# Optimization experiments

Hardware: AMD Instinct MI355X
Metric: run time of the kernel (lower is better)

The kernel has to match this reference:

```python
import jax, jax.numpy as jnp
import numpy as np

EPS = 1e-5  # torch BatchNorm1d default

def _silu(x):
    return x * jax.nn.sigmoid(x)

def _bn(x, g, b, rm, rv, axis):
    # eval-mode batchnorm along given channel axis
    shape = [1] * x.ndim
    shape[axis] = -1
    return (x - rm.reshape(shape)) * (g.reshape(shape) / jnp.sqrt(rv.reshape(shape) + EPS)) + b.reshape(shape)

def setup_inputs() -> dict:
    key = jax.random.key(0)
    ks = jax.random.split(key, 12)
    b, n, p, d, r = 64, 256, 12, 128, 2
    x = jax.random.normal(ks[0], (b, n, p, d), dtype=jnp.float32)
    # k branch: Conv1d(p -> 1, k=1, bias=False) + BN(1)
    wk = jax.random.normal(ks[1], (p,), dtype=jnp.float32) / np.sqrt(p)
    bn_k_g = jax.random.uniform(ks[2], (1,), dtype=jnp.float32, minval=0.5, maxval=1.5)
    bn_k_b = 0.1 * jax.random.normal(ks[3], (1,), dtype=jnp.float32)
    bn_k_rm = jnp.zeros((1,), jnp.float32)
    bn_k_rv = jnp.ones((1,), jnp.float32)
    # v branch: Conv1d(d -> d, k=1, bias=False) + BN(d)
    wv = jax.random.normal(ks[4], (d, d), dtype=jnp.float32) / np.sqrt(d)
    bn_v_g = jax.random.uniform(ks[5], (d,), dtype=jnp.float32, minval=0.5, maxval=1.5)
    bn_v_b = 0.1 * jax.random.normal(ks[6], (d,), dtype=jnp.float32)
    bn_v_rm = jnp.zeros((d,), jnp.float32)
    bn_v_rv = jnp.ones((d,), jnp.float32)
    # fc_avg / fc_max: Linear(n, n//r, bias=False) -> GELU -> Linear(n//r, n, bias=False)
    w_avg1 = jax.random.normal(ks[7], (n // r, n), dtype=jnp.float32) / np.sqrt(n)
    w_avg2 = jax.random.normal(ks[8], (n, n // r), dtype=jnp.float32) / np.sqrt(n // r)
    w_max1 = jax.random.normal(ks[9], (n // r, n), dtype=jnp.float32) / np.sqrt(n)
    w_max2 = jax.random.normal(ks[10], (n, n // r), dtype=jnp.float32) / np.sqrt(n // r)
    return dict(x=x, wk=wk, bn_k_g=bn_k_g, bn_k_b=bn_k_b, bn_k_rm=bn_k_rm, bn_k_rv=bn_k_rv,
                wv=wv, bn_v_g=bn_v_g, bn_v_b=bn_v_b, bn_v_rm=bn_v_rm, bn_v_rv=bn_v_rv,
                w_avg1=w_avg1, w_avg2=w_avg2, w_max1=w_max1, w_max2=w_max2)

def _forward(x, wk, bn_k_g, bn_k_b, bn_k_rm, bn_k_rv, wv, bn_v_g, bn_v_b, bn_v_rm, bn_v_rv,
             w_avg1, w_avg2, w_max1, w_max2):
    b, n, p, d = x.shape
    xf = x.reshape(b * n, p, d)
    # squeeze-excite gates: pool over d, FC over n
    avg = jnp.mean(xf, axis=-1).reshape(b, n, p).transpose(0, 2, 1)  # [b,p,n]
    mx = jnp.max(xf, axis=-1).reshape(b, n, p).transpose(0, 2, 1)    # [b,p,n]
    gelu = lambda t: jax.nn.gelu(t, approximate=False)
    avg_g = jax.nn.sigmoid(gelu(avg @ w_avg1.T) @ w_avg2.T).transpose(0, 2, 1)  # [b,n,p]
    max_g = jax.nn.sigmoid(gelu(mx @ w_max1.T) @ w_max2.T).transpose(0, 2, 1)   # [b,n,p]
    # k: 1x1 conv over p channels -> [bn, d], BN(1ch), SiLU, softmax over d
    k_raw = jnp.einsum('bpd,p->bd', xf, wk)
    k = jax.nn.softmax(_silu(k_raw * (bn_k_g / jnp.sqrt(bn_k_rv + EPS)) - bn_k_rm * (bn_k_g / jnp.sqrt(bn_k_rv + EPS)) + bn_k_b), axis=-1)  # [bn,d]
    # v: 1x1 conv over d channels on [bn,d,p], BN(d), SiLU -> [bn,p,d]
    v_raw = jnp.einsum('bpd,ed->bpe', xf, wv)  # channel axis is last here
    v = _silu(_bn(v_raw, bn_v_g, bn_v_b, bn_v_rm, bn_v_rv, axis=2))  # [bn,p,d]
    # y = v @ k : [bn,p];  y_pool = (max+avg) @ v : [bn,d]
    y = jnp.einsum('bpd,bd->bp', v, k)
    pool = (max_g + avg_g).reshape(b * n, p)
    y_pool = jnp.einsum('bp,bpd->bd', pool, v)
    out = y_pool[:, None, :] * y[:, :, None]  # [bn,p,d]
    return out.reshape(b, n, p, d)

def reference(x, wk, bn_k_g, bn_k_b, bn_k_rm, bn_k_rv, wv, bn_v_g, bn_v_b, bn_v_rm, bn_v_rv,
              w_avg1, w_avg2, w_max1, w_max2):
    return _forward(x, wk, bn_k_g, bn_k_b, bn_k_rm, bn_k_rv, wv, bn_v_g, bn_v_b, bn_v_rm, bn_v_rv,
                    w_avg1, w_avg2, w_max1, w_max2)
```

## Files before the change

### kernel.cpp

```cpp
#include <hip/hip_runtime.h>
#include <hip/hip_bf16.h>

#define B_   64
#define N_   256
#define P_   12
#define D_   128
#define BN_  (B_*N_)
#define EPSV 1e-5f

typedef float  f32x4  __attribute__((ext_vector_type(4)));
typedef __bf16 bf16x8 __attribute__((ext_vector_type(8)));
typedef __bf16 bf16x4 __attribute__((ext_vector_type(4)));

__device__ float  g_avg[768*256];
__device__ float  g_mx [768*256];
__device__ float  g_h1 [1536*128];
__device__ float  g_pool[BN_*P_];
__device__ float  g_k  [BN_*D_];
__device__ __bf16 g_xbf[(size_t)BN_*P_*D_];
__device__ __align__(16) __bf16 g_wvbf[128*128];
__device__ float  g_tv [128];

__device__ inline float sigm_(float x) { return 1.0f / (1.0f + __expf(-x)); }

__device__ inline float dot4_(float4 a, float4 b, float acc) {
  acc = fmaf(a.x, b.x, acc); acc = fmaf(a.y, b.y, acc);
  acc = fmaf(a.z, b.z, acc); acc = fmaf(a.w, b.w, acc);
  return acc;
}

__global__ __launch_bounds__(256) void k0_prep(const float* __restrict__ wv,
                                               const float* __restrict__ vg,
                                               const float* __restrict__ vb,
                                               const float* __restrict__ vrm,
                                               const float* __restrict__ vrv) {
  int t = blockIdx.x * 256 + threadIdx.x;
  if (blockIdx.x == 0 && threadIdx.x < 128) {
    float s0 = vg[threadIdx.x] * rsqrtf(vrv[threadIdx.x] + EPSV);
    g_tv[threadIdx.x] = vb[threadIdx.x] - vrm[threadIdx.x] * s0;
  }
  int idx = t * 4;
  int e = idx >> 7, d0 = idx & 127;
  float s = vg[e] * rsqrtf(vrv[e] + EPSV);
  bf16x4 h;
#pragma unroll
  for (int j = 0; j < 4; ++j) h[j] = (__bf16)(wv[e * 128 + d0 + j] * s);
  *(bf16x4*)(g_wvbf + idx) = h;
}

__global__ __launch_bounds__(256) void k1_pool(const float* __restrict__ x,
                                               const float* __restrict__ wk,
                                               const float* __restrict__ kg,
                                               const float* __restrict__ kb,
                                               const float* __restrict__ krm,
                                               const float* __restrict__ krv) {
  int w = threadIdx.x >> 6, l = threadIdx.x & 63;
  int bn = blockIdx.x * 4 + w;
  const float* xp = x + (size_t)bn * (P_ * D_);
  __bf16* xbp = g_xbf + (size_t)bn * (P_ * D_);
  int half = l >> 5, lane32 = l & 31;
  float ksc = kg[0] * rsqrtf(krv[0] + EPSV);
  float kbs = kb[0] - krm[0] * ksc;
  float s6[6], m6[6];
  float kr0 = 0, kr1 = 0, kr2 = 0, kr3 = 0;
#pragma unroll
  for (int pp = 0; pp < 6; ++pp) {
    int p = pp * 2 + half;
    float4 v = *(const float4*)(xp + p * D_ + lane32 * 4);
    bf16x4 h;
    h[0] = (__bf16)v.x; h[1] = (__bf16)v.y; h[2] = (__bf16)v.z; h[3] = (__bf16)v.w;
    *(bf16x4*)(xbp + p * D_ + lane32 * 4) = h;
    float wkp = wk[p];
    kr0 = fmaf(v.x, wkp, kr0); kr1 = fmaf(v.y, wkp, kr1);
    kr2 = fmaf(v.z, wkp, kr2); kr3 = fmaf(v.w, wkp, kr3);
    float s = (v.x + v.y) + (v.z + v.w);
    float m = fmaxf(fmaxf(v.x, v.y), fmaxf(v.z, v.w));
#pragma unroll
    for (int off = 16; off; off >>= 1) {
      s += __shfl_xor(s, off);
      m = fmaxf(m, __shfl_xor(m, off));
    }
    s6[pp] = s * (1.0f / D_);
    m6[pp] = m;
  }
  kr0 += __shfl_xor(kr0, 32); kr1 += __shfl_xor(kr1, 32);
  kr2 += __shfl_xor(kr2, 32); kr3 += __shfl_xor(kr3, 32);
  float z0 = kr0 * ksc + kbs, z1 = kr1 * ksc + kbs;
  float z2 = kr2 * ksc + kbs, z3 = kr3 * ksc + kbs;
  z0 = z0 * sigm_(z0); z1 = z1 * sigm_(z1);
  z2 = z2 * sigm_(z2); z3 = z3 * sigm_(z3);
  float mx = fmaxf(fmaxf(z0, z1), fmaxf(z2, z3));
#pragma unroll
  for (int off = 16; off; off >>= 1) mx = fmaxf(mx, __shfl_xor(mx, off));
  float e0 = __expf(z0 - mx), e1 = __expf(z1 - mx);
  float e2 = __expf(z2 - mx), e3 = __expf(z3 - mx);
  float es = (e0 + e1) + (e2 + e3);
#pragma unroll
  for (int off = 16; off; off >>= 1) es += __shfl_xor(es, off);
  float inv = 1.0f / es;
  if (half == 0) {
    float4 kk; kk.x = e0 * inv; kk.y = e1 * inv; kk.z = e2 * inv; kk.w = e3 * inv;
    *(float4*)(g_k + (size_t)bn * D_ + lane32 * 4) = kk;
  }
  if (lane32 == 0) {
    int b = bn >> 8, n = bn & 255;
#pragma unroll
    for (int pp = 0; pp < 6; ++pp) {
      int p = pp * 2 + half;
      g_avg[(b * P_ + p) * N_ + n] = s6[pp];
      g_mx [(b * P_ + p) * N_ + n] = m6[pp];
    }
  }
}

__global__ __launch_bounds__(256) void k2_l1(const float* __restrict__ w_avg1,
                                             const float* __restrict__ w_max1) {
  __shared__ float in_t[16 * 256];
  __shared__ float w_t[64 * 68];
  int t = threadIdx.x;
  int rblk = blockIdx.x % 96, cblk = blockIdx.x / 96;
  int rr0 = rblk * 16, c0 = cblk * 64;
  bool mxb = (rr0 >= 768);
  int r768 = mxb ? rr0 - 768 : rr0;
  const float* in = (mxb ? g_mx : g_avg) + (size_t)r768 * 256;
  const float* w1 = mxb ? w_max1 : w_avg1;
#pragma unroll
  for (int i = 0; i < 4; ++i) {
    int F = t + i * 256, r = F >> 6, k4 = F & 63;
    *(float4*)(in_t + r * 256 + k4 * 4) = *(const float4*)(in + r * 256 + k4 * 4);
  }
  int c = t & 63, rq = t >> 6;
  float a0 = 0, a1 = 0, a2 = 0, a3 = 0;
  for (int kc = 0; kc < 4; ++kc) {
    __syncthreads();
#pragma unroll
    for (int i = 0; i < 4; ++i) {
      int F = t + i * 256, cr = F >> 4, k4 = F & 15;
      *(float4*)(w_t + cr * 68 + k4 * 4) =
          *(const float4*)(w1 + (size_t)(c0 + cr) * 256 + kc * 64 + k4 * 4);
    }
    __syncthreads();
#pragma unroll
    for (int k4 = 0; k4 < 16; ++k4) {
      float4 wv4 = *(float4*)(w_t + c * 68 + k4 * 4);
      a0 = dot4_(*(float4*)(in_t + (rq * 4 + 0) * 256 + kc * 64 + k4 * 4), wv4, a0);
      a1 = dot4_(*(float4*)(in_t + (rq * 4 + 1) * 256 + kc * 64 + k4 * 4), wv4, a1);
      a2 = dot4_(*(float4*)(in_t + (rq * 4 + 2) * 256 + kc * 64 + k4 * 4), wv4, a2);
      a3 = dot4_(*(float4*)(in_t + (rq * 4 + 3) * 256 + kc * 64 + k4 * 4), wv4, a3);
    }
  }
  float accs[4] = {a0, a1, a2, a3};
#pragma unroll
  for (int r = 0; r < 4; ++r) {
    float a = accs[r];
    float g = 0.5f * a * (1.0f + erff(a * 0.70710678f));
    g_h1[(size_t)(rr0 + rq * 4 + r) * 128 + c0 + c] = g;
  }
}

__global__ __launch_bounds__(256) void k2_l2(const float* __restrict__ w_avg2,
                                             const float* __restrict__ w_max2) {
  __shared__ float ina_t[16 * 128];
  __shared__ float inm_t[16 * 128];
  __shared__ float wa_t[64 * 68];
  __shared__ float wm_t[64 * 68];
  int t = threadIdx.x;
  int rblk = blockIdx.x % 48, cblk = blockIdx.x / 48;
  int rr0 = rblk * 16, n0 = cblk * 64;
#pragma unroll
  for (int i = 0; i < 2; ++i) {
    int F = t + i * 256, r = F >> 5, k4 = F & 31;
    *(float4*)(ina_t + r * 128 + k4 * 4) = *(const float4*)(g_h1 + (size_t)(rr0 + r) * 128 + k4 * 4);
    *(float4*)(inm_t + r * 128 + k4 * 4) = *(const float4*)(g_h1 + (size_t)(768 + rr0 + r) * 128 + k4 * 4);
  }
  int c = t & 63, rq = t >> 6;
  float aa0=0, aa1=0, aa2=0, aa3=0, am0=0, am1=0, am2=0, am3=0;
  for (int kc = 0; kc < 2; ++kc) {
    __syncthreads();
#pragma unroll
    for (int i = 0; i < 4; ++i) {
      int F = t + i * 256, cr = F >> 4, k4 = F & 15;
      *(float4*)(wa_t + cr * 68 + k4 * 4) =
          *(const float4*)(w_avg2 + (size_t)(n0 + cr) * 128 + kc * 64 + k4 * 4);
      *(float4*)(wm_t + cr * 68 + k4 * 4) =
          *(const float4*)(w_max2 + (size_t)(n0 + cr) * 128 + kc * 64 + k4 * 4);
    }
    __syncthreads();
#pragma unroll
    for (int k4 = 0; k4 < 16; ++k4) {
      float4 wa4 = *(float4*)(wa_t + c * 68 + k4 * 4);
      float4 wm4 = *(float4*)(wm_t + c * 68 + k4 * 4);
      float4 i0 = *(float4*)(ina_t + (rq * 4 + 0) * 128 + kc * 64 + k4 * 4);
      float4 i1 = *(float4*)(ina_t + (rq * 4 + 1) * 128 + kc * 64 + k4 * 4);
      float4 i2 = *(float4*)(ina_t + (rq * 4 + 2) * 128 + kc * 64 + k4 * 4);
      float4 i3 = *(float4*)(ina_t + (rq * 4 + 3) * 128 + kc * 64 + k4 * 4);
      aa0 = dot4_(i0, wa4, aa0); aa1 = dot4_(i1, wa4, aa1);
      aa2 = dot4_(i2, wa4, aa2); aa3 = dot4_(i3, wa4, aa3);
      float4 j0 = *(float4*)(inm_t + (rq * 4 + 0) * 128 + kc * 64 + k4 * 4);
      float4 j1 = *(float4*)(inm_t + (rq * 4 + 1) * 128 + kc * 64 + k4 * 4);
      float4 j2 = *(float4*)(inm_t + (rq * 4 + 2) * 128 + kc * 64 + k4 * 4);
      float4 j3 = *(float4*)(inm_t + (rq * 4 + 3) * 128 + kc * 64 + k4 * 4);
      am0 = dot4_(j0, wm4, am0); am1 = dot4_(j1, wm4, am1);
      am2 = dot4_(j2, wm4, am2); am3 = dot4_(j3, wm4, am3);
    }
  }
  float va[4] = {aa0, aa1, aa2, aa3};
  float vm[4] = {am0, am1, am2, am3};
#pragma unroll
  for (int r = 0; r < 4; ++r) {
    int rr = rr0 + rq * 4 + r;
    int b = rr / 12, p = rr % 12;
    float pv = sigm_(va[r]) + sigm_(vm[r]);
    g_pool[((size_t)b * 256 + (n0 + c)) * 12 + p] = pv;
  }
}

__global__ __launch_bounds__(64) void k3_main(float* __restrict__ out) {
  int l = threadIdx.x;
  int bcol = l & 15;
  int arow = bcol > 11 ? 11 : bcol;
  int ak = (l >> 4) * 8;
  int p0 = (l >> 4) * 4;
  bool rows_ok = (p0 < 12);

  bf16x8 bfr[8][4];
#pragma unroll
  for (int nt = 0; nt < 8; ++nt) {
    const __bf16* wp = g_wvbf + (bcol + nt * 16) * 128 + ak;
#pragma unroll
    for (int ks = 0; ks < 4; ++ks)
      bfr[nt][ks] = *(const bf16x8*)(wp + ks * 32);
  }
  float tv_e[8];
#pragma unroll
  for (int nt = 0; nt < 8; ++nt) tv_e[nt] = g_tv[bcol + nt * 16];

  for (int it = 0; it < 4; ++it) {
    int bn = blockIdx.x * 4 + it;

    const __bf16* xp = g_xbf + (size_t)bn * (P_ * D_) + arow * D_;
    bf16x8 afr[4];
#pragma unroll
    for (int ks = 0; ks < 4; ++ks) afr[ks] = *(const bf16x8*)(xp + ks * 32 + ak);
    const float* kp = g_k + (size_t)bn * D_;
    float k_e[8];
#pragma unroll
    for (int nt = 0; nt < 8; ++nt) k_e[nt] = kp[bcol + nt * 16];
    float pool_r[4] = {0.f, 0.f, 0.f, 0.f};
    if (rows_ok) {
      const float* pp = g_pool + (size_t)bn * 12 + p0;
#pragma unroll
      for (int r = 0; r < 4; ++r) pool_r[r] = pp[r];
    }

    float y_r[4] = {0.f, 0.f, 0.f, 0.f};
    float ypp[8];
#pragma unroll
    for (int nt = 0; nt < 8; ++nt) {
      f32x4 acc = (f32x4){0.f, 0.f, 0.f, 0.f};
#pragma unroll
      for (int ks = 0; ks < 4; ++ks)
        acc = __builtin_amdgcn_mfma_f32_16x16x32_bf16(afr[ks], bfr[nt][ks], acc, 0, 0, 0);
      float tvv = tv_e[nt];
      float s = 0.f;
#pragma unroll
      for (int r = 0; r < 4; ++r) {
        float a = acc[r] + tvv;
        float v = a * sigm_(a);
        y_r[r] = fmaf(v, k_e[nt], y_r[r]);
        s = fmaf(pool_r[r], v, s);
      }
      ypp[nt] = s;
    }

#pragma unroll
    for (int r = 0; r < 4; ++r) {
#pragma unroll
      for (int off = 8; off; off >>= 1) y_r[r] += __shfl_xor(y_r[r], off);
    }
#pragma unroll
    for (int nt = 0; nt < 8; ++nt) {
      ypp[nt] += __shfl_xor(ypp[nt], 16);
      ypp[nt] += __shfl_xor(ypp[nt], 32);
    }

    int cs = (l & 7) * 2;
    int ntw = l >> 3;
    float ypx = 0.f, ypy = 0.f;
#pragma unroll
    for (int nt = 0; nt < 8; ++nt) {
      float sx = __shfl(ypp[nt], cs);
      float sy = __shfl(ypp[nt], cs + 1);
      ypx = (ntw == nt) ? sx : ypx;
      ypy = (ntw == nt) ? sy : ypy;
    }

    float* op = out + (size_t)bn * (P_ * D_);
#pragma unroll
    for (int p = 0; p < P_; ++p) {
      float yp = __shfl(y_r[p & 3], (p >> 2) * 16);
      float2 o;
      o.x = yp * ypx;
      o.y = yp * ypy;
      *(float2*)(op + p * 128 + 2 * l) = o;
    }
  }
}

extern "C" void kernel_launch(void* const* d_in, const int* in_sizes, int n_in,
                              void* d_out, int out_size, void* d_ws, size_t ws_size,
                              hipStream_t stream) {
  const float* x   = (const float*)d_in[0];
  const float* wk  = (const float*)d_in[1];
  const float* kg  = (const float*)d_in[2];
  const float* kbb = (const float*)d_in[3];
  const float* krm = (const float*)d_in[4];
  const float* krv = (const float*)d_in[5];
  const float* wvp = (const float*)d_in[6];
  const float* vg  = (const float*)d_in[7];
  const float* vbb = (const float*)d_in[8];
  const float* vrm = (const float*)d_in[9];
  const float* vrv = (const float*)d_in[10];
  const float* wa1 = (const float*)d_in[11];
  const float* wa2 = (const float*)d_in[12];
  const float* wm1 = (const float*)d_in[13];
  const float* wm2 = (const float*)d_in[14];
  float* out = (float*)d_out;

  k0_prep<<<16, 256, 0, stream>>>(wvp, vg, vbb, vrm, vrv);
  k1_pool<<<4096, 256, 0, stream>>>(x, wk, kg, kbb, krm, krv);
  k2_l1<<<192, 256, 0, stream>>>(wa1, wm1);
  k2_l2<<<192, 256, 0, stream>>>(wa2, wm2);
  k3_main<<<4096, 64, 0, stream>>>(out);
}
```

Before: 111.0 us.

## Move V projection GEMM into pooling kernel and store activated V in bf16

Fuses the bf16 MFMA V-projection, BN, SiLU and the y = v·k reduction into the pooling pass over x, using a swizzled LDS copy of the folded weights. Softmax k now stays in LDS, so the separate bf16 copy of x and the k buffer are gone. The final kernel only reads the stored activated V and y to form the pooled output product. The trade-off is that the stored V intermediate is larger than the old bf16 x copy, and every block reloads the 32KB weight matrix into LDS.

```diff
diff --git a/kernel.cpp b/kernel.cpp
--- a/kernel.cpp
+++ b/kernel.cpp
@@ -16,8 +16,8 @@
 __device__ float  g_mx [768*256];
 __device__ float  g_h1 [1536*128];
 __device__ float  g_pool[BN_*P_];
-__device__ float  g_k  [BN_*D_];
-__device__ __bf16 g_xbf[(size_t)BN_*P_*D_];
+__device__ float  g_y  [BN_*P_];
+__device__ __bf16 g_v  [(size_t)BN_*8*64*4];
 __device__ __align__(16) __bf16 g_wvbf[128*128];
 __device__ float  g_tv [128];
 
@@ -39,13 +39,17 @@
     float s0 = vg[threadIdx.x] * rsqrtf(vrv[threadIdx.x] + EPSV);
     g_tv[threadIdx.x] = vb[threadIdx.x] - vrm[threadIdx.x] * s0;
   }
-  int idx = t * 4;
-  int e = idx >> 7, d0 = idx & 127;
+  int e = t >> 5;
   float s = vg[e] * rsqrtf(vrv[e] + EPSV);
+  int qbase = t * 8;
+  int swz = (e & 7) << 4;
   bf16x4 h;
 #pragma unroll
-  for (int j = 0; j < 4; ++j) h[j] = (__bf16)(wv[e * 128 + d0 + j] * s);
-  *(bf16x4*)(g_wvbf + idx) = h;
+  for (int j = 0; j < 4; ++j) {
+    int inner = ((qbase & 255) + j * 2) ^ swz;
+    h[j] = (__bf16)(wv[e * 128 + (inner >> 1)] * s);
+  }
+  *(bf16x4*)((char*)g_wvbf + qbase) = h;
 }
 
 __global__ __launch_bounds__(256) void k1_pool(const float* __restrict__ x,
@@ -54,61 +58,130 @@
                                                const float* __restrict__ kb,
                                                const float* __restrict__ krm,
                                                const float* __restrict__ krv) {
-  int w = threadIdx.x >> 6, l = threadIdx.x & 63;
-  int bn = blockIdx.x * 4 + w;
-  const float* xp = x + (size_t)bn * (P_ * D_);
-  __bf16* xbp = g_xbf + (size_t)bn * (P_ * D_);
-  int half = l >> 5, lane32 = l & 31;
+  __shared__ __align__(16) __bf16 wv_lds[128 * 128];
+  __shared__ float k_lds[4][128];
+
+  int t = threadIdx.x, w = t >> 6, l = t & 63;
+  {
+    const uint4* src = (const uint4*)g_wvbf;
+    uint4* dst = (uint4*)wv_lds;
+#pragma unroll
+    for (int i = 0; i < 8; ++i) dst[i * 256 + t] = src[i * 256 + t];
+  }
   float ksc = kg[0] * rsqrtf(krv[0] + EPSV);
   float kbs = kb[0] - krm[0] * ksc;
-  float s6[6], m6[6];
-  float kr0 = 0, kr1 = 0, kr2 = 0, kr3 = 0;
-#pragma unroll
-  for (int pp = 0; pp < 6; ++pp) {
-    int p = pp * 2 + half;
-    float4 v = *(const float4*)(xp + p * D_ + lane32 * 4);
-    bf16x4 h;
-    h[0] = (__bf16)v.x; h[1] = (__bf16)v.y; h[2] = (__bf16)v.z; h[3] = (__bf16)v.w;
-    *(bf16x4*)(xbp + p * D_ + lane32 * 4) = h;
-    float wkp = wk[p];
-    kr0 = fmaf(v.x, wkp, kr0); kr1 = fmaf(v.y, wkp, kr1);
-    kr2 = fmaf(v.z, wkp, kr2); kr3 = fmaf(v.w, wkp, kr3);
-    float s = (v.x + v.y) + (v.z + v.w);
-    float m = fmaxf(fmaxf(v.x, v.y), fmaxf(v.z, v.w));
-#pragma unroll
-    for (int off = 16; off; off >>= 1) {
-      s += __shfl_xor(s, off);
-      m = fmaxf(m, __shfl_xor(m, off));
-    }
-    s6[pp] = s * (1.0f / D_);
-    m6[pp] = m;
-  }
-  kr0 += __shfl_xor(kr0, 32); kr1 += __shfl_xor(kr1, 32);
-  kr2 += __shfl_xor(kr2, 32); kr3 += __shfl_xor(kr3, 32);
-  float z0 = kr0 * ksc + kbs, z1 = kr1 * ksc + kbs;
-  float z2 = kr2 * ksc + kbs, z3 = kr3 * ksc + kbs;
-  z0 = z0 * sigm_(z0); z1 = z1 * sigm_(z1);
-  z2 = z2 * sigm_(z2); z3 = z3 * sigm_(z3);
-  float mx = fmaxf(fmaxf(z0, z1), fmaxf(z2, z3));
-#pragma unroll
-  for (int off = 16; off; off >>= 1) mx = fmaxf(mx, __shfl_xor(mx, off));
-  float e0 = __expf(z0 - mx), e1 = __expf(z1 - mx);
-  float e2 = __expf(z2 - mx), e3 = __expf(z3 - mx);
-  float es = (e0 + e1) + (e2 + e3);
-#pragma unroll
-  for (int off = 16; off; off >>= 1) es += __shfl_xor(es, off);
-  float inv = 1.0f / es;
-  if (half == 0) {
-    float4 kk; kk.x = e0 * inv; kk.y = e1 * inv; kk.z = e2 * inv; kk.w = e3 * inv;
-    *(float4*)(g_k + (size_t)bn * D_ + lane32 * 4) = kk;
-  }
-  if (lane32 == 0) {
-    int b = bn >> 8, n = bn & 255;
+  __syncthreads();
+
+  int half = l >> 5, lane32 = l & 31;
+  int bcol = l & 15;
+  int arow = bcol > 11 ? 11 : bcol;
+  int ak = (l >> 4) * 8;
+  int bko = (l >> 4) * 16;
+  int p0 = (l >> 4) * 4;
+  bool rows_ok = (p0 < 12);
+  float tv_e[8];
+#pragma unroll
+  for (int nt = 0; nt < 8; ++nt) tv_e[nt] = g_tv[bcol + nt * 16];
+
+  for (int it = 0; it < 2; ++it) {
+    int bn = blockIdx.x * 8 + it * 4 + w;
+    const float* xp = x + (size_t)bn * (P_ * D_);
+
+    float s6[6], m6[6];
+    float kr0 = 0, kr1 = 0, kr2 = 0, kr3 = 0;
 #pragma unroll
     for (int pp = 0; pp < 6; ++pp) {
       int p = pp * 2 + half;
-      g_avg[(b * P_ + p) * N_ + n] = s6[pp];
-      g_mx [(b * P_ + p) * N_ + n] = m6[pp];
+      float4 v = *(const float4*)(xp + p * D_ + lane32 * 4);
+      float wkp = wk[p];
+      kr0 = fmaf(v.x, wkp, kr0); kr1 = fmaf(v.y, wkp, kr1);
+      kr2 = fmaf(v.z, wkp, kr2); kr3 = fmaf(v.w, wkp, kr3);
+      float s = (v.x + v.y) + (v.z + v.w);
+      float m = fmaxf(fmaxf(v.x, v.y), fmaxf(v.z, v.w));
+#pragma unroll
+      for (int off = 16; off; off >>= 1) {
+        s += __shfl_xor(s, off);
+        m = fmaxf(m, __shfl_xor(m, off));
+      }
+      s6[pp] = s * (1.0f / D_);
+      m6[pp] = m;
+    }
+    if (lane32 == 0) {
+      int b = bn >> 8, n = bn & 255;
+#pragma unroll
+      for (int pp = 0; pp < 6; ++pp) {
+        int p = pp * 2 + half;
+        g_avg[(b * P_ + p) * N_ + n] = s6[pp];
+        g_mx [(b * P_ + p) * N_ + n] = m6[pp];
+      }
+    }
+    kr0 += __shfl_xor(kr0, 32); kr1 += __shfl_xor(kr1, 32);
+    kr2 += __shfl_xor(kr2, 32); kr3 += __shfl_xor(kr3, 32);
+    float z0 = kr0 * ksc + kbs, z1 = kr1 * ksc + kbs;
+    float z2 = kr2 * ksc + kbs, z3 = kr3 * ksc + kbs;
+    z0 = z0 * sigm_(z0); z1 = z1 * sigm_(z1);
+    z2 = z2 * sigm_(z2); z3 = z3 * sigm_(z3);
+    float mx = fmaxf(fmaxf(z0, z1), fmaxf(z2, z3));
+#pragma unroll
+    for (int off = 16; off; off >>= 1) mx = fmaxf(mx, __shfl_xor(mx, off));
+    float e0 = __expf(z0 - mx), e1 = __expf(z1 - mx);
+    float e2 = __expf(z2 - mx), e3 = __expf(z3 - mx);
+    float es = (e0 + e1) + (e2 + e3);
+#pragma unroll
+    for (int off = 16; off; off >>= 1) es += __shfl_xor(es, off);
+    float inv = 1.0f / es;
+    if (half == 0) {
+      float4 kk; kk.x = e0 * inv; kk.y = e1 * inv; kk.z = e2 * inv; kk.w = e3 * inv;
+      *(float4*)(&k_lds[w][lane32 * 4]) = kk;
+    }
+    float k_e[8];
+#pragma unroll
+    for (int nt = 0; nt < 8; ++nt) k_e[nt] = k_lds[w][bcol + nt * 16];
+
+    bf16x8 afr[4];
+#pragma unroll
+    for (int ks = 0; ks < 4; ++ks) {
+      const float* src = xp + arow * 128 + ks * 32 + ak;
+      float4 lo = *(const float4*)(src);
+      float4 hi = *(const float4*)(src + 4);
+      bf16x8 a;
+      a[0] = (__bf16)lo.x; a[1] = (__bf16)lo.y; a[2] = (__bf16)lo.z; a[3] = (__bf16)lo.w;
+      a[4] = (__bf16)hi.x; a[5] = (__bf16)hi.y; a[6] = (__bf16)hi.z; a[7] = (__bf16)hi.w;
+      afr[ks] = a;
+    }
+    float y_r[4] = {0.f, 0.f, 0.f, 0.f};
+    __bf16* vp = g_v + ((size_t)bn * 8) * 256 + l * 4;
+#pragma unroll
+    for (int nt = 0; nt < 8; ++nt) {
+      int er = bcol + nt * 16;
+      int base = er * 256;
+      int sw = (er & 7) << 4;
+      f32x4 acc = (f32x4){0.f, 0.f, 0.f, 0.f};
+#pragma unroll
+      for (int ks = 0; ks < 4; ++ks) {
+        int byte = (base + ks * 64 + bko) ^ sw;
+        bf16x8 bfr = *(const bf16x8*)((const char*)wv_lds + byte);
+        acc = __builtin_amdgcn_mfma_f32_16x16x32_bf16(afr[ks], bfr, acc, 0, 0, 0);
+      }
+      float tvv = tv_e[nt];
+      bf16x4 vb;
+#pragma unroll
+      for (int r = 0; r < 4; ++r) {
+        float a = acc[r] + tvv;
+        float v = a * sigm_(a);
+        y_r[r] = fmaf(v, k_e[nt], y_r[r]);
+        vb[r] = (__bf16)v;
+      }
+      *(bf16x4*)(vp + nt * 256) = vb;
+    }
+#pragma unroll
+    for (int r = 0; r < 4; ++r) {
+#pragma unroll
+      for (int off = 8; off; off >>= 1) y_r[r] += __shfl_xor(y_r[r], off);
+    }
+    if (bcol == 0 && rows_ok) {
+      float4 yq; yq.x = y_r[0]; yq.y = y_r[1]; yq.z = y_r[2]; yq.w = y_r[3];
+      *(float4*)(g_y + (size_t)bn * 12 + p0) = yq;
     }
   }
 }
@@ -217,93 +290,52 @@
 
 __global__ __launch_bounds__(64) void k3_main(float* __restrict__ out) {
   int l = threadIdx.x;
-  int bcol = l & 15;
-  int arow = bcol > 11 ? 11 : bcol;
-  int ak = (l >> 4) * 8;
+  int bn = blockIdx.x;
   int p0 = (l >> 4) * 4;
   bool rows_ok = (p0 < 12);
 
-  bf16x8 bfr[8][4];
+  float pool_r[4] = {0.f, 0.f, 0.f, 0.f};
+  if (rows_ok) {
+    const float* pp = g_pool + (size_t)bn * 12 + p0;
+#pragma unroll
+    for (int r = 0; r < 4; ++r) pool_r[r] = pp[r];
+  }
+
+  const __bf16* vp = g_v + ((size_t)bn * 8) * 256 + l * 4;
+  float ypp[8];
 #pragma unroll
   for (int nt = 0; nt < 8; ++nt) {
-    const __bf16* wp = g_wvbf + (bcol + nt * 16) * 128 + ak;
-#pragma unroll
-    for (int ks = 0; ks < 4; ++ks)
-      bfr[nt][ks] = *(const bf16x8*)(wp + ks * 32);
-  }
-  float tv_e[8];
-#pragma unroll
-  for (int nt = 0; nt < 8; ++nt) tv_e[nt] = g_tv[bcol + nt * 16];
-
-  for (int it = 0; it < 4; ++it) {
-    int bn = blockIdx.x * 4 + it;
-
-    const __bf16* xp = g_xbf + (size_t)bn * (P_ * D_) + arow * D_;
-    bf16x8 afr[4];
-#pragma unroll
-    for (int ks = 0; ks < 4; ++ks) afr[ks] = *(const bf16x8*)(xp + ks * 32 + ak);
-    const float* kp = g_k + (size_t)bn * D_;
-    float k_e[8];
-#pragma unroll
-    for (int nt = 0; nt < 8; ++nt) k_e[nt] = kp[bcol + nt * 16];
-    float pool_r[4] = {0.f, 0.f, 0.f, 0.f};
-    if (rows_ok) {
-      const float* pp = g_pool + (size_t)bn * 12 + p0;
-#pragma unroll
-      for (int r = 0; r < 4; ++r) pool_r[r] = pp[r];
-    }
-
-    float y_r[4] = {0.f, 0.f, 0.f, 0.f};
-    float ypp[8];
-#pragma unroll
-    for (int nt = 0; nt < 8; ++nt) {
-      f32x4 acc = (f32x4){0.f, 0.f, 0.f, 0.f};
-#pragma unroll
-      for (int ks = 0; ks < 4; ++ks)
-        acc = __builtin_amdgcn_mfma_f32_16x16x32_bf16(afr[ks], bfr[nt][ks], acc, 0, 0, 0);
-      float tvv = tv_e[nt];
-      float s = 0.f;
-#pragma unroll
-      for (int r = 0; r < 4; ++r) {
-        float a = acc[r] + tvv;
-        float v = a * sigm_(a);
-        y_r[r] = fmaf(v, k_e[nt], y_r[r]);
-        s = fmaf(pool_r[r], v, s);
-      }
-      ypp[nt] = s;
-    }
-
-#pragma unroll
-    for (int r = 0; r < 4; ++r) {
-#pragma unroll
-      for (int off = 8; off; off >>= 1) y_r[r] += __shfl_xor(y_r[r], off);
-    }
-#pragma unroll
-    for (int nt = 0; nt < 8; ++nt) {
-      ypp[nt] += __shfl_xor(ypp[nt], 16);
-      ypp[nt] += __shfl_xor(ypp[nt], 32);
-    }
-
-    int cs = (l & 7) * 2;
-    int ntw = l >> 3;
-    float ypx = 0.f, ypy = 0.f;
-#pragma unroll
-    for (int nt = 0; nt < 8; ++nt) {
-      float sx = __shfl(ypp[nt], cs);
-      float sy = __shfl(ypp[nt], cs + 1);
-      ypx = (ntw == nt) ? sx : ypx;
-      ypy = (ntw == nt) ? sy : ypy;
-    }
-
-    float* op = out + (size_t)bn * (P_ * D_);
-#pragma unroll
-    for (int p = 0; p < P_; ++p) {
-      float yp = __shfl(y_r[p & 3], (p >> 2) * 16);
-      float2 o;
-      o.x = yp * ypx;
-      o.y = yp * ypy;
-      *(float2*)(op + p * 128 + 2 * l) = o;
-    }
+    bf16x4 vb = *(const bf16x4*)(vp + nt * 256);
+    float s = 0.f;
+#pragma unroll
+    for (int r = 0; r < 4; ++r) s = fmaf(pool_r[r], (float)vb[r], s);
+    ypp[nt] = s;
+  }
+#pragma unroll
+  for (int nt = 0; nt < 8; ++nt) {
+    ypp[nt] += __shfl_xor(ypp[nt], 16);
+    ypp[nt] += __shfl_xor(ypp[nt], 32);
+  }
+  int cs = (l & 7) * 2;
+  int ntw = l >> 3;
+  float ypx = 0.f, ypy = 0.f;
+#pragma unroll
+  for (int nt = 0; nt < 8; ++nt) {
+    float sx = __shfl(ypp[nt], cs);
+    float sy = __shfl(ypp[nt], cs + 1);
+    ypx = (ntw == nt) ? sx : ypx;
+    ypy = (ntw == nt) ? sy : ypy;
+  }
+
+  const float* yb = g_y + (size_t)bn * 12;
+  float* op = out + (size_t)bn * (P_ * D_);
+#pragma unroll
+  for (int p = 0; p < P_; ++p) {
+    float yp = yb[p];
+    float2 o;
+    o.x = yp * ypx;
+    o.y = yp * ypy;
+    *(float2*)(op + p * 128 + 2 * l) = o;
   }
 }
 
@@ -328,8 +360,8 @@
   float* out = (float*)d_out;
 
   k0_prep<<<16, 256, 0, stream>>>(wvp, vg, vbb, vrm, vrv);
-  k1_pool<<<4096, 256, 0, stream>>>(x, wk, kg, kbb, krm, krv);
+  k1_pool<<<2048, 256, 0, stream>>>(x, wk, kg, kbb, krm, krv);
   k2_l1<<<192, 256, 0, stream>>>(wa1, wm1);
   k2_l2<<<192, 256, 0, stream>>>(wa2, wm2);
-  k3_main<<<4096, 64, 0, stream>>>(out);
-}
+  k3_main<<<16384, 64, 0, stream>>>(out);
+}
```

Result: slower. 122.4 us (+10.3%).
